# Kernel optimization log

Hardware: AMD Instinct MI355X
Metric: run time of the kernel (lower is better)

The kernel has to match this reference:

```python
import jax, jax.numpy as jnp
import numpy as np

B, CIN, HID, T, W, H, TAU = 8, 16, 64, 4, 32, 32, 5
EPS = 1e-5
DN = ('NCDHW', 'OIDHW', 'NCDHW')


def conv3d(x, w, b):
    # 'same' conv3d, NCDHW layout
    y = jax.lax.conv_general_dilated(x, w, (1, 1, 1), 'SAME', dimension_numbers=DN)
    return y + b[None, :, None, None, None]


def ln3(u):
    # F.layer_norm over the last 3 (spatial) dims, no affine
    mu = jnp.mean(u, axis=(-3, -2, -1), keepdims=True)
    var = jnp.var(u, axis=(-3, -2, -1), keepdims=True)
    return (u - mu) * jax.lax.rsqrt(var + EPS)


def ln4(u, w, b):
    # nn.LayerNorm(memory_shape): over last 4 dims (C,T,W,H), with affine
    mu = jnp.mean(u, axis=(-4, -3, -2, -1), keepdims=True)
    var = jnp.var(u, axis=(-4, -3, -2, -1), keepdims=True)
    return (u - mu) * jax.lax.rsqrt(var + EPS) * w + b


def self_attention(r, c_history):
    scale = 1.0 / np.sqrt(T * W * H)
    scores = jnp.einsum('bctwh,lbctwh->bl', r, c_history) * scale  # [B, TAU]
    # faithful to source: softmax over dim=0 (the batch axis of the [b,l] scores)
    attn = jax.nn.softmax(scores, axis=0)
    return jnp.einsum('bl,lbctwh->bctwh', attn, c_history)


def setup_inputs() -> dict:
    key = jax.random.key(0)
    ks = jax.random.split(key, 8)
    x = jax.random.normal(ks[0], (B, CIN, T, W, H), jnp.float32)
    c_history = jax.random.normal(ks[1], (TAU, B, HID, T, W, H), jnp.float32)
    m = jax.random.normal(ks[2], (B, HID, T, W, H), jnp.float32)
    h = jax.random.normal(ks[3], (B, HID, T, W, H), jnp.float32)
    Wx = jax.random.normal(ks[4], (7, HID, CIN, 3, 3, 3), jnp.float32) * 0.05
    bx = jnp.zeros((7, HID), jnp.float32)
    # 9 state-branch conv kernels: [hr, hi, hg, mi', mg', mf', ho, co, mo]
    Wh = jax.random.normal(ks[5], (9, HID, HID, 3, 3, 3), jnp.float32) * 0.02
    bh = jnp.zeros((9, HID), jnp.float32)
    w111 = jax.random.normal(ks[6], (HID, 2 * HID, 1, 1, 1), jnp.float32) * 0.05
    b111 = jnp.zeros((HID,), jnp.float32)
    ln_w = jnp.ones((HID, T, W, H), jnp.float32)
    ln_b = jnp.zeros((HID, T, W, H), jnp.float32)
    return dict(x=x, c_history=c_history, m=m, h=h, Wx=Wx, bx=bx, Wh=Wh, bh=bh,
                w111=w111, b111=b111, ln_w=ln_w, ln_b=ln_b)


def reference(x, c_history, m, h, Wx, bx, Wh, bh, w111, b111, ln_w, ln_b):
    cx = lambda i: conv3d(x, Wx[i], bx[i])
    cs = lambda u, i: conv3d(u, Wh[i], bh[i])
    r = jax.nn.sigmoid(ln3(cx(0) + cs(h, 0)))
    i = jax.nn.sigmoid(ln3(cx(1) + cs(h, 1)))
    g = jnp.tanh(ln3(cx(2) + cs(h, 2)))
    recall = self_attention(r, c_history)
    c = i * g + ln4(c_history[-1] + recall, ln_w, ln_b)
    i_p = jax.nn.sigmoid(ln3(cx(3) + cs(m, 3)))
    g_p = jnp.tanh(ln3(cx(4) + cs(m, 4)))
    f_p = jax.nn.sigmoid(ln3(cx(5) + cs(m, 5)))
    m_new = i_p * g_p + f_p * m
    o = jax.nn.sigmoid(ln3(cx(6) + cs(h, 6) + cs(c, 7) + cs(m_new, 8)))
    h_new = o * jnp.tanh(conv3d(jnp.concatenate([c, m_new], axis=1), w111, b111))
    c_history_new = jnp.concatenate([c_history[1:], c[None]], axis=0)
    return (c_history_new, m_new, h_new)
```

## Files before the change

kernel.cpp:

```cpp
#include <hip/hip_runtime.h>
#include <hip/hip_bf16.h>
#include <math.h>

#define BATCH 8
#define CIN 16
#define HID 64
#define S2 1024
#define SP 4096
#define CHB 262144
#define TAU 5
#define GATE_SZ 2097152
#define EPS 1e-5f

#define WS_Z_OFF   ((size_t)3 * GATE_SZ)
#define WS_ST_OFF  ((size_t)4 * GATE_SZ)

typedef unsigned short u16;
typedef __attribute__((ext_vector_type(8))) short  short8;
typedef __attribute__((ext_vector_type(8))) u16    ushort8;
typedef __attribute__((ext_vector_type(4))) float  f32x4;

#define N7 (7*27*64*96)
#define NO (27*64*128)
#define N1 (64*128)

__device__ __forceinline__ u16 f2b(float v) {
    __hip_bfloat16 h = __float2bfloat16(v);
    u16 r; __builtin_memcpy(&r, &h, 2); return r;
}

__device__ __forceinline__ float* gate_ptr(float* out, float* ws, int g) {
    return (g < 4) ? (out + (size_t)g * GATE_SZ) : (ws + (size_t)(g - 4) * GATE_SZ);
}

__device__ __forceinline__ float fsig(float v) {
    v = fminf(fmaxf(v, -30.f), 30.f);
    return 1.f / (1.f + __expf(-v));
}
__device__ __forceinline__ float ftanh(float v) {
    v = fminf(fmaxf(v, -15.f), 15.f);
    const float t = __expf(-2.f * v);
    return (1.f - t) / (1.f + t);
}

__global__ __launch_bounds__(256) void pack_w_k(const float* __restrict__ Wx,
                                                const float* __restrict__ Wh,
                                                const float* __restrict__ w111,
                                                u16* __restrict__ A7, u16* __restrict__ Ao,
                                                u16* __restrict__ A111,
                                                float* __restrict__ stats)
{
    if (blockIdx.x == 0 && threadIdx.x < 128) stats[threadIdx.x] = 0.f;
    const int idx = blockIdx.x * 256 + threadIdx.x;
    if (idx < N7) {
        const int k = idx % 96, oc = (idx / 96) % 64, tap = (idx / (96*64)) % 27, g = idx / (96*64*27);
        float v = 0.f;
        if (k < 16)      v = Wx[((size_t)(g*64 + oc)*16 + k)      * 27 + tap];
        else if (k < 80) v = Wh[((size_t)(g*64 + oc)*64 + (k-16)) * 27 + tap];
        A7[idx] = f2b(v);
    } else if (idx < N7 + NO) {
        const int j = idx - N7;
        const int k = j % 128, oc = (j / 128) % 64, tap = j / (128*64);
        float v = (k < 64) ? Wh[((size_t)(7*64 + oc)*64 + k)      * 27 + tap]
                           : Wh[((size_t)(8*64 + oc)*64 + (k-64)) * 27 + tap];
        Ao[j] = f2b(v);
    } else if (idx < N7 + NO + N1) {
        const int j = idx - N7 - NO;
        A111[j] = f2b(w111[j]);
    }
}

__global__ __launch_bounds__(256) void pack_xhm_k(const float* __restrict__ x,
                                                  const float* __restrict__ h,
                                                  const float* __restrict__ m,
                                                  u16* __restrict__ XH, u16* __restrict__ XM)
{
    __shared__ float t[144][65];
    const int bi = blockIdx.x, b = bi >> 6, s0 = (bi & 63) << 6;
    for (int i = threadIdx.x; i < 144*64; i += 256) {
        const int row = i >> 6, sc = i & 63;
        float v;
        if (row < 16)      v = x[((size_t)b*16 + row)      * SP + s0 + sc];
        else if (row < 80) v = h[((size_t)b*64 + (row-16)) * SP + s0 + sc];
        else               v = m[((size_t)b*64 + (row-80)) * SP + s0 + sc];
        t[row][sc] = v;
    }
    __syncthreads();
    for (int j = threadIdx.x; j < 64*96; j += 256) {
        const int s = j / 96, ch = j % 96;
        const size_t o = ((size_t)b*4096 + s0 + s) * 96 + ch;
        XH[o] = f2b(ch < 80 ? t[ch][s] : 0.f);
        XM[o] = f2b(ch < 16 ? t[ch][s] : (ch < 80 ? t[ch + 64][s] : 0.f));
    }
}

__device__ __forceinline__ int swz32(int r, int c) {
    return r * 32 + ((c ^ ((r >> 1) & 3)) << 3);
}

template<int KCH, int TAPS, int NR, int MODE, int MT, int MINW>
__global__ __launch_bounds__(256, MINW) void conv_mfma_k(
    const u16* __restrict__ XA, const u16* __restrict__ XB,
    const u16* __restrict__ Apack,
    const float* __restrict__ bxp, const float* __restrict__ bhp,
    const float* __restrict__ b111,
    float* __restrict__ out, float* __restrict__ ws)
{
    constexpr int YT   = NR + 2;
    constexpr int ROWS = 4 * YT * 34;
    __shared__ __align__(16) u16 xs[ROWS * 32];

    const int bi = blockIdx.x;
    int g = 0, b, y0, ocb = 0, kc_lo = 0, kc_hi = KCH / 32;
    const u16* X; const u16* Ag; float* outp;
    if (MODE == 0) {
        constexpr int YB = 32 / NR;
        ocb = (bi & 1) * 32;
        const int r2 = bi >> 1;
        g  = r2 / (8 * YB);
        b  = (r2 / YB) % 8;
        y0 = (r2 % YB) * NR;
        X  = (g >= 3 && g <= 5) ? XB : XA;
        Ag = Apack + (size_t)g * TAPS * 64 * KCH;
        outp = gate_ptr(out, ws, g) + (size_t)b * CHB;
    } else if (MODE == 1) {
        b = bi >> 5; y0 = bi & 31;
        X = XA; Ag = Apack;
        outp = ws + (size_t)2 * GATE_SZ + (size_t)b * CHB;
    } else {
        b = bi >> 5; y0 = bi & 31;
        X = XA; Ag = Apack;
        outp = ws + (size_t)b * CHB;
    }
    const u16* Xb = X + (size_t)b * 4096 * KCH;

    const int tid  = threadIdx.x;
    const int w    = tid >> 6;
    const int lane = tid & 63;
    const int xn   = lane & 15, quad = lane >> 4;

    f32x4 acc[MT][2 * NR] = {};

    for (int kc = kc_lo; kc < kc_hi; ++kc) {
        if (kc != kc_lo) __syncthreads();
        for (int cix = tid; cix < ROWS * 4; cix += 256) {
            const int r = cix >> 2, sub = cix & 3;
            const int t = r / (YT * 34), rem = r % (YT * 34);
            const int yy = rem / 34, xx = rem % 34;
            const int gy = y0 + yy - 1, gx = xx - 1;
            ushort8 v = {0, 0, 0, 0, 0, 0, 0, 0};
            if ((unsigned)gy < 32u && (unsigned)gx < 32u)
                v = *(const ushort8*)&Xb[(size_t)(t * 1024 + gy * 32 + gx) * KCH + kc * 32 + sub * 8];
            *(ushort8*)&xs[swz32(r, sub)] = v;
        }
        __syncthreads();

        if (TAPS == 27) {
            const int kd_lo = (w == 0) ? 1 : 0;
            const int kd_hi = (w == 3) ? 2 : 3;
            for (int kd = kd_lo; kd < kd_hi; ++kd) {
                const int tin  = w + kd - 1;
                const int rowt = tin * YT * 34;
                #pragma unroll
                for (int jj = 0; jj < 9; ++jj) {
                    const int ky = jj / 3, kx = jj % 3;
                    short8 a[MT], bf[2 * NR];
                    #pragma unroll
                    for (int mt = 0; mt < MT; ++mt)
                        a[mt] = *(const short8*)
                            &Ag[(size_t)((kd * 9 + jj) * 64 + ocb + mt * 16 + xn) * KCH + kc * 32 + quad * 8];
                    #pragma unroll
                    for (int nt = 0; nt < 2 * NR; ++nt) {
                        const int ysub = nt >> 1, xh = nt & 1;
                        const int row = rowt + (ysub + ky) * 34 + xh * 16 + xn + kx;
                        bf[nt] = *(const short8*)&xs[swz32(row, quad)];
                    }
                    #pragma unroll
                    for (int nt = 0; nt < 2 * NR; ++nt)
                        #pragma unroll
                        for (int mt = 0; mt < MT; ++mt)
                            acc[mt][nt] = __builtin_amdgcn_mfma_f32_16x16x32_bf16(a[mt], bf[nt], acc[mt][nt], 0, 0, 0);
                }
            }
        } else {
            short8 a[MT], bf[2 * NR];
            #pragma unroll
            for (int mt = 0; mt < MT; ++mt)
                a[mt] = *(const short8*)&Ag[(size_t)(mt * 16 + xn) * KCH + kc * 32 + quad * 8];
            #pragma unroll
            for (int nt = 0; nt < 2 * NR; ++nt) {
                const int ysub = nt >> 1, xh = nt & 1;
                const int row = (w * YT + ysub + 1) * 34 + xh * 16 + xn + 1;
                bf[nt] = *(const short8*)&xs[swz32(row, quad)];
            }
            #pragma unroll
            for (int nt = 0; nt < 2 * NR; ++nt)
                #pragma unroll
                for (int mt = 0; mt < MT; ++mt)
                    acc[mt][nt] = __builtin_amdgcn_mfma_f32_16x16x32_bf16(a[mt], bf[nt], acc[mt][nt], 0, 0, 0);
        }
    }

    #pragma unroll
    for (int mt = 0; mt < MT; ++mt)
    #pragma unroll
    for (int nt = 0; nt < 2 * NR; ++nt) {
        const int ysub = nt >> 1, xh = nt & 1;
        const int sp = w * 1024 + (y0 + ysub) * 32 + xh * 16 + xn;
        #pragma unroll
        for (int reg = 0; reg < 4; ++reg) {
            const int oc = ocb + mt * 16 + quad * 4 + reg;
            float bias;
            if (MODE == 0)      bias = bxp[g * 64 + oc] + bhp[g * 64 + oc];
            else if (MODE == 1) bias = bhp[7 * 64 + oc] + bhp[8 * 64 + oc];
            else                bias = b111[oc];
            float* p = outp + (size_t)oc * SP + sp;
            float vv = acc[mt][nt][reg] + bias;
            if (MODE == 1) vv += *p;
            *p = vv;
        }
    }
}

__global__ __launch_bounds__(256) void ln3_stats_k(float* __restrict__ out,
                                                   float* __restrict__ ws,
                                                   float* __restrict__ lnstats)
{
    const int blk = blockIdx.x;
    const int g = blk >> 9;
    const float* p = gate_ptr(out, ws, g) + (size_t)(blk & 511) * SP;
    const int tid = threadIdx.x;

    float s = 0.f, s2 = 0.f;
    for (int k = tid; k < SP; k += 256) { float v = p[k]; s += v; s2 += v * v; }
    #pragma unroll
    for (int off = 32; off > 0; off >>= 1) { s += __shfl_down(s, off); s2 += __shfl_down(s2, off); }
    __shared__ float rs[4], rs2[4];
    if ((tid & 63) == 0) { rs[tid >> 6] = s; rs2[tid >> 6] = s2; }
    __syncthreads();
    if (tid == 0) {
        float S  = rs[0] + rs[1] + rs[2] + rs[3];
        float Sq = rs2[0] + rs2[1] + rs2[2] + rs2[3];
        float mu  = S * (1.f / SP);
        float var = Sq * (1.f / SP) - mu * mu;
        lnstats[2 * blk]     = mu;
        lnstats[2 * blk + 1] = rsqrtf(var + EPS);
    }
}

__global__ __launch_bounds__(256) void ln3_act_k(float* __restrict__ out,
                                                 float* __restrict__ ws, int gate0)
{
    const int blk = blockIdx.x;
    const int g = gate0 + (blk >> 9);
    float* p = gate_ptr(out, ws, g) + (size_t)(blk & 511) * SP;
    const int tid = threadIdx.x;

    float s = 0.f, s2 = 0.f;
    for (int k = tid; k < SP; k += 256) { float v = p[k]; s += v; s2 += v * v; }
    #pragma unroll
    for (int off = 32; off > 0; off >>= 1) { s += __shfl_down(s, off); s2 += __shfl_down(s2, off); }
    __shared__ float rs[4], rs2[4], stat[2];
    if ((tid & 63) == 0) { rs[tid >> 6] = s; rs2[tid >> 6] = s2; }
    __syncthreads();
    if (tid == 0) {
        float S  = rs[0] + rs[1] + rs[2] + rs[3];
        float Sq = rs2[0] + rs2[1] + rs2[2] + rs2[3];
        float mu  = S * (1.f / SP);
        float var = Sq * (1.f / SP) - mu * mu;
        stat[0] = mu; stat[1] = rsqrtf(var + EPS);
    }
    __syncthreads();
    const float mu = stat[0], r = stat[1];
    for (int k = tid; k < SP; k += 256)
        p[k] = fsig((p[k] - mu) * r);
}

__global__ __launch_bounds__(256) void scores_k(const float* __restrict__ u0,
                                                const float* __restrict__ chist,
                                                const float* __restrict__ lnstats,
                                                float* __restrict__ stats)
{
    const int blk = blockIdx.x;
    const int b = blk >> 6, chn = blk & 63;
    const float mu = lnstats[2 * (b * 64 + chn)];
    const float rr = lnstats[2 * (b * 64 + chn) + 1];
    const float* rp = u0 + (size_t)b * CHB;
    const int lo = chn * SP;
    float s[TAU] = {};
    for (int k = lo + threadIdx.x; k < lo + SP; k += 256) {
        const float rv = fsig((rp[k] - mu) * rr);
        #pragma unroll
        for (int l = 0; l < TAU; ++l) s[l] += rv * chist[(size_t)(l * BATCH + b) * CHB + k];
    }
    __shared__ float rsh[TAU][4];
    #pragma unroll
    for (int l = 0; l < TAU; ++l) {
        float v = s[l];
        #pragma unroll
        for (int off = 32; off > 0; off >>= 1) v += __shfl_down(v, off);
        if ((threadIdx.x & 63) == 0) rsh[l][threadIdx.x >> 6] = v;
    }
    __syncthreads();
    if (threadIdx.x < TAU) {
        const int l = threadIdx.x;
        atomicAdd(&stats[l * 8 + b],
                  (rsh[l][0] + rsh[l][1] + rsh[l][2] + rsh[l][3]) * (1.f / 64.f));
    }
}

__global__ __launch_bounds__(256) void recall_k(const float* __restrict__ chist,
                                                float* __restrict__ ws,
                                                float* __restrict__ part)
{
    const float* stats = ws + WS_ST_OFF;
    const int blk = blockIdx.x;
    const int b = blk >> 10;
    const int idx = (blk & 1023) * 256 + threadIdx.x;

    __shared__ float attn[TAU];
    if (threadIdx.x < TAU) {
        const int l = threadIdx.x;
        float mx = -1e30f;
        for (int bb = 0; bb < BATCH; ++bb) mx = fmaxf(mx, stats[l * 8 + bb]);
        float sum = 0.f, e = 0.f;
        for (int bb = 0; bb < BATCH; ++bb) {
            float t = __expf(stats[l * 8 + bb] - mx);
            sum += t;
            if (bb == b) e = t;
        }
        attn[l] = e / sum;
    }
    __syncthreads();
    const float a0 = attn[0], a1 = attn[1], a2 = attn[2], a3 = attn[3], a4 = attn[4];

    const size_t e = (size_t)b * CHB + idx;
    const size_t LB = (size_t)BATCH * CHB;
    float z = chist[4 * LB + e] * (1.f + a4)
            + a0 * chist[0 * LB + e] + a1 * chist[1 * LB + e]
            + a2 * chist[2 * LB + e] + a3 * chist[3 * LB + e];
    ws[WS_Z_OFF + e] = z;

    float s = z, s2 = z * z;
    #pragma unroll
    for (int off = 32; off > 0; off >>= 1) { s += __shfl_down(s, off); s2 += __shfl_down(s2, off); }
    __shared__ float rs[4], rs2[4];
    if ((threadIdx.x & 63) == 0) { rs[threadIdx.x >> 6] = s; rs2[threadIdx.x >> 6] = s2; }
    __syncthreads();
    if (threadIdx.x == 0) {
        part[blk]        = rs[0] + rs[1] + rs[2] + rs[3];
        part[8192 + blk] = rs2[0] + rs2[1] + rs2[2] + rs2[3];
    }
}

__global__ __launch_bounds__(256) void cm_pcm_k(float* __restrict__ out, float* __restrict__ ws,
                                                const float* __restrict__ m,
                                                const float* __restrict__ lnw,
                                                const float* __restrict__ lnb,
                                                const float* __restrict__ part,
                                                const float* __restrict__ lnstats,
                                                u16* __restrict__ PCM)
{
    __shared__ __align__(16) u16 tl[64][136];
    __shared__ float lst[5][64][2];
    const int bi = blockIdx.x;
    const int b = bi >> 6;
    const int s0 = (bi & 63) << 6;

    for (int j = threadIdx.x; j < 5 * 64; j += 256) {
        const int gg = j >> 6, chn = j & 63;
        lst[gg][chn][0] = lnstats[2 * ((gg + 1) * 512 + b * 64 + chn)];
        lst[gg][chn][1] = lnstats[2 * ((gg + 1) * 512 + b * 64 + chn) + 1];
    }
    float s = 0.f, s2 = 0.f;
    for (int j = threadIdx.x; j < 1024; j += 256) {
        s  += part[b * 1024 + j];
        s2 += part[8192 + b * 1024 + j];
    }
    #pragma unroll
    for (int off = 32; off > 0; off >>= 1) { s += __shfl_down(s, off); s2 += __shfl_down(s2, off); }
    __shared__ float rs[4], rs2[4], st[2];
    if ((threadIdx.x & 63) == 0) { rs[threadIdx.x >> 6] = s; rs2[threadIdx.x >> 6] = s2; }
    __syncthreads();
    if (threadIdx.x == 0) {
        float S  = rs[0] + rs[1] + rs[2] + rs[3];
        float Sq = rs2[0] + rs2[1] + rs2[2] + rs2[3];
        float mu  = S * (1.f / CHB);
        float var = Sq * (1.f / CHB) - mu * mu;
        st[0] = mu; st[1] = rsqrtf(var + EPS);
    }
    __syncthreads();
    const float mu = st[0], rstd = st[1];

    for (int i = threadIdx.x; i < 1024; i += 256) {
        const int chn = i >> 4;
        const int sp4 = (i & 15) << 2;
        const size_t e = (size_t)b * CHB + (size_t)chn * SP + s0 + sp4;
        const size_t le = (size_t)chn * SP + s0 + sp4;
        float4 z  = *(const float4*)&ws[WS_Z_OFF + e];
        float4 u1 = *(const float4*)&gate_ptr(out, ws, 1)[e];
        float4 u2 = *(const float4*)&gate_ptr(out, ws, 2)[e];
        float4 u3 = *(const float4*)&gate_ptr(out, ws, 3)[e];
        float4 u4 = *(const float4*)&gate_ptr(out, ws, 4)[e];
        float4 u5 = *(const float4*)&gate_ptr(out, ws, 5)[e];
        float4 mm = *(const float4*)&m[e];
        float4 lw = *(const float4*)&lnw[le];
        float4 lb = *(const float4*)&lnb[le];
        const float m1 = lst[0][chn][0], r1 = lst[0][chn][1];
        const float m2 = lst[1][chn][0], r2 = lst[1][chn][1];
        const float m3 = lst[2][chn][0], r3 = lst[2][chn][1];
        const float m4 = lst[3][chn][0], r4 = lst[3][chn][1];
        const float m5 = lst[4][chn][0], r5 = lst[4][chn][1];
        float4 c, mn;
        {
            const float uu1[4] = {u1.x, u1.y, u1.z, u1.w};
            const float uu2[4] = {u2.x, u2.y, u2.z, u2.w};
            const float uu3[4] = {u3.x, u3.y, u3.z, u3.w};
            const float uu4[4] = {u4.x, u4.y, u4.z, u4.w};
            const float uu5[4] = {u5.x, u5.y, u5.z, u5.w};
            const float zz[4]  = {z.x, z.y, z.z, z.w};
            const float mmv[4] = {mm.x, mm.y, mm.z, mm.w};
            const float lwv[4] = {lw.x, lw.y, lw.z, lw.w};
            const float lbv[4] = {lb.x, lb.y, lb.z, lb.w};
            float cv[4], mv[4];
            #pragma unroll
            for (int k = 0; k < 4; ++k) {
                const float gi = fsig ((uu1[k] - m1) * r1);
                const float gg = ftanh((uu2[k] - m2) * r2);
                const float ip = fsig ((uu3[k] - m3) * r3);
                const float gp = ftanh((uu4[k] - m4) * r4);
                const float fp = fsig ((uu5[k] - m5) * r5);
                cv[k] = gi * gg + (zz[k] - mu) * rstd * lwv[k] + lbv[k];
                mv[k] = ip * gp + fp * mmv[k];
                tl[sp4 + k][chn]      = f2b(cv[k]);
                tl[sp4 + k][64 + chn] = f2b(mv[k]);
            }
            c.x = cv[0]; c.y = cv[1]; c.z = cv[2]; c.w = cv[3];
            mn.x = mv[0]; mn.y = mv[1]; mn.z = mv[2]; mn.w = mv[3];
        }
        *(float4*)&out[(size_t)4 * GATE_SZ + e] = c;
        *(float4*)&out[(size_t)5 * GATE_SZ + e] = mn;
    }
    __syncthreads();
    for (int j = threadIdx.x; j < 1024; j += 256) {
        const int sidx = j >> 4, c8 = (j & 15) << 3;
        ushort8 v = *(const ushort8*)&tl[sidx][c8];
        *(ushort8*)&PCM[((size_t)b * 4096 + s0 + sidx) * 128 + c8] = v;
    }
}

__global__ __launch_bounds__(256) void tail_k(const float* __restrict__ chist,
                                              const float* __restrict__ o,
                                              const float* __restrict__ v,
                                              float* __restrict__ out)
{
    const int bi = blockIdx.x;
    if (bi < 8192) {
        const size_t i = (size_t)bi * 256 + threadIdx.x;
        ((float4*)out)[i] = ((const float4*)(chist + GATE_SZ))[i];
    } else {
        const size_t i = (size_t)(bi - 8192) * 256 + threadIdx.x;
        float4 ov = ((const float4*)o)[i], vv = ((const float4*)v)[i];
        float4 r;
        r.x = ov.x * ftanh(vv.x); r.y = ov.y * ftanh(vv.y);
        r.z = ov.z * ftanh(vv.z); r.w = ov.w * ftanh(vv.w);
        ((float4*)(out + (size_t)6 * GATE_SZ))[i] = r;
    }
}

extern "C" void kernel_launch(void* const* d_in, const int* in_sizes, int n_in,
                              void* d_out, int out_size, void* d_ws, size_t ws_size,
                              hipStream_t stream)
{
    const float* x    = (const float*)d_in[0];
    const float* ch   = (const float*)d_in[1];
    const float* m    = (const float*)d_in[2];
    const float* h    = (const float*)d_in[3];
    const float* Wx   = (const float*)d_in[4];
    const float* bx   = (const float*)d_in[5];
    const float* Wh   = (const float*)d_in[6];
    const float* bh   = (const float*)d_in[7];
    const float* w111 = (const float*)d_in[8];
    const float* b111 = (const float*)d_in[9];
    const float* lnw  = (const float*)d_in[10];
    const float* lnb  = (const float*)d_in[11];
    float* out = (float*)d_out;
    float* ws  = (float*)d_ws;

    u16* XH   = (u16*)(out + (size_t)4 * GATE_SZ);
    u16* A7   = (u16*)(out + (size_t)5 * GATE_SZ);
    u16* XM   = (u16*)(out + (size_t)6 * GATE_SZ);
    u16* Ao   = XM + (size_t)BATCH * 4096 * 96;
    u16* A111 = Ao + (size_t)NO;
    u16* PCM  = (u16*)out;
    float* part    = (float*)(A111 + N1);
    float* lnstats = part + 16384;
    float* stats   = ws + WS_ST_OFF;

    pack_w_k<<<(N7 + NO + N1 + 255) / 256, 256, 0, stream>>>(Wx, Wh, w111, A7, Ao, A111, stats);
    pack_xhm_k<<<512, 256, 0, stream>>>(x, h, m, XH, XM);

    conv_mfma_k<96, 27, 2, 0, 2, 4><<<1792, 256, 0, stream>>>(XH, XM, A7, bx, bh, nullptr, out, ws);
    ln3_stats_k<<<3072, 256, 0, stream>>>(out, ws, lnstats);

    scores_k<<<512, 256, 0, stream>>>(out, ch, lnstats, stats);
    recall_k<<<8192, 256, 0, stream>>>(ch, ws, part);
    cm_pcm_k<<<512, 256, 0, stream>>>(out, ws, m, lnw, lnb, part, lnstats, PCM);

    conv_mfma_k<128, 27, 1, 1, 4, 3><<<256, 256, 0, stream>>>(PCM, nullptr, Ao, nullptr, bh, nullptr, out, ws);
    ln3_act_k<<<512, 256, 0, stream>>>(out, ws, 6);
    conv_mfma_k<128, 1, 1, 2, 4, 3><<<256, 256, 0, stream>>>(PCM, nullptr, A111, nullptr, nullptr, b111, out, ws);

    tail_k<<<10240, 256, 0, stream>>>(ch, ws + (size_t)2 * GATE_SZ, ws, out);
}
```

Before: 392.1 us.

## Fuse LN3 stats into conv epilogue via atomics and double-buffer tap loads

```diff
diff --git a/kernel.cpp b/kernel.cpp
--- a/kernel.cpp
+++ b/kernel.cpp
@@ -48,10 +48,12 @@
                                                 const float* __restrict__ w111,
                                                 u16* __restrict__ A7, u16* __restrict__ Ao,
                                                 u16* __restrict__ A111,
-                                                float* __restrict__ stats)
-{
-    if (blockIdx.x == 0 && threadIdx.x < 128) stats[threadIdx.x] = 0.f;
+                                                float* __restrict__ stats,
+                                                float* __restrict__ sums)
+{
     const int idx = blockIdx.x * 256 + threadIdx.x;
+    if (idx < 128)  stats[idx] = 0.f;
+    if (idx < 6144) sums[idx] = 0.f;
     if (idx < N7) {
         const int k = idx % 96, oc = (idx / 96) % 64, tap = (idx / (96*64)) % 27, g = idx / (96*64*27);
         float v = 0.f;
@@ -104,7 +106,8 @@
     const u16* __restrict__ Apack,
     const float* __restrict__ bxp, const float* __restrict__ bhp,
     const float* __restrict__ b111,
-    float* __restrict__ out, float* __restrict__ ws)
+    float* __restrict__ out, float* __restrict__ ws,
+    float* __restrict__ sums)
 {
     constexpr int YT   = NR + 2;
     constexpr int ROWS = 4 * YT * 34;
@@ -155,49 +158,48 @@
         }
         __syncthreads();
 
-        if (TAPS == 27) {
-            const int kd_lo = (w == 0) ? 1 : 0;
-            const int kd_hi = (w == 3) ? 2 : 3;
-            for (int kd = kd_lo; kd < kd_hi; ++kd) {
-                const int tin  = w + kd - 1;
-                const int rowt = tin * YT * 34;
-                #pragma unroll
-                for (int jj = 0; jj < 9; ++jj) {
-                    const int ky = jj / 3, kx = jj % 3;
-                    short8 a[MT], bf[2 * NR];
-                    #pragma unroll
-                    for (int mt = 0; mt < MT; ++mt)
-                        a[mt] = *(const short8*)
-                            &Ag[(size_t)((kd * 9 + jj) * 64 + ocb + mt * 16 + xn) * KCH + kc * 32 + quad * 8];
-                    #pragma unroll
-                    for (int nt = 0; nt < 2 * NR; ++nt) {
-                        const int ysub = nt >> 1, xh = nt & 1;
-                        const int row = rowt + (ysub + ky) * 34 + xh * 16 + xn + kx;
-                        bf[nt] = *(const short8*)&xs[swz32(row, quad)];
-                    }
-                    #pragma unroll
-                    for (int nt = 0; nt < 2 * NR; ++nt)
-                        #pragma unroll
-                        for (int mt = 0; mt < MT; ++mt)
-                            acc[mt][nt] = __builtin_amdgcn_mfma_f32_16x16x32_bf16(a[mt], bf[nt], acc[mt][nt], 0, 0, 0);
-                }
-            }
-        } else {
-            short8 a[MT], bf[2 * NR];
+        auto load_ab = [&](short8* a, short8* bf, int kd_, int ky_, int kx_) {
+            const int tap = (TAPS == 27) ? (kd_ * 9 + ky_ * 3 + kx_) : 0;
             #pragma unroll
             for (int mt = 0; mt < MT; ++mt)
-                a[mt] = *(const short8*)&Ag[(size_t)(mt * 16 + xn) * KCH + kc * 32 + quad * 8];
+                a[mt] = *(const short8*)
+                    &Ag[(size_t)(tap * 64 + ocb + mt * 16 + xn) * KCH + kc * 32 + quad * 8];
+            const int rowt = (w + kd_ - 1) * YT * 34;
             #pragma unroll
             for (int nt = 0; nt < 2 * NR; ++nt) {
                 const int ysub = nt >> 1, xh = nt & 1;
-                const int row = (w * YT + ysub + 1) * 34 + xh * 16 + xn + 1;
+                const int row = rowt + (ysub + ky_) * 34 + xh * 16 + xn + kx_;
                 bf[nt] = *(const short8*)&xs[swz32(row, quad)];
             }
+        };
+        auto do_mfma = [&](short8* a, short8* bf) {
             #pragma unroll
             for (int nt = 0; nt < 2 * NR; ++nt)
                 #pragma unroll
                 for (int mt = 0; mt < MT; ++mt)
                     acc[mt][nt] = __builtin_amdgcn_mfma_f32_16x16x32_bf16(a[mt], bf[nt], acc[mt][nt], 0, 0, 0);
+        };
+
+        if (TAPS == 27) {
+            int kd = (w == 0) ? 1 : 0;
+            const int kd_hi = (w == 3) ? 2 : 3;
+            const int ntap = (kd_hi - kd) * 9;
+            int ky = 0, kx = 0;
+            auto adv = [&]() { if (++kx == 3) { kx = 0; if (++ky == 3) { ky = 0; ++kd; } } };
+
+            short8 a0[MT], b0[2 * NR], a1[MT], b1[2 * NR];
+            load_ab(a0, b0, kd, ky, kx);
+            for (int t = 0; t + 2 <= ntap; t += 2) {
+                adv(); load_ab(a1, b1, kd, ky, kx);
+                do_mfma(a0, b0);
+                if (t + 3 <= ntap) { adv(); load_ab(a0, b0, kd, ky, kx); }
+                do_mfma(a1, b1);
+            }
+            if (ntap & 1) do_mfma(a0, b0);
+        } else {
+            short8 a0[MT], b0[2 * NR];
+            load_ab(a0, b0, 1, 1, 1);
+            do_mfma(a0, b0);
         }
     }
 
@@ -220,31 +222,31 @@
             *p = vv;
         }
     }
-}
-
-__global__ __launch_bounds__(256) void ln3_stats_k(float* __restrict__ out,
-                                                   float* __restrict__ ws,
-                                                   float* __restrict__ lnstats)
-{
-    const int blk = blockIdx.x;
-    const int g = blk >> 9;
-    const float* p = gate_ptr(out, ws, g) + (size_t)(blk & 511) * SP;
-    const int tid = threadIdx.x;
-
-    float s = 0.f, s2 = 0.f;
-    for (int k = tid; k < SP; k += 256) { float v = p[k]; s += v; s2 += v * v; }
-    #pragma unroll
-    for (int off = 32; off > 0; off >>= 1) { s += __shfl_down(s, off); s2 += __shfl_down(s2, off); }
-    __shared__ float rs[4], rs2[4];
-    if ((tid & 63) == 0) { rs[tid >> 6] = s; rs2[tid >> 6] = s2; }
-    __syncthreads();
-    if (tid == 0) {
-        float S  = rs[0] + rs[1] + rs[2] + rs[3];
-        float Sq = rs2[0] + rs2[1] + rs2[2] + rs2[3];
-        float mu  = S * (1.f / SP);
-        float var = Sq * (1.f / SP) - mu * mu;
-        lnstats[2 * blk]     = mu;
-        lnstats[2 * blk + 1] = rsqrtf(var + EPS);
+
+    if (MODE == 0 && g < 6) {
+        #pragma unroll
+        for (int mt = 0; mt < MT; ++mt)
+        #pragma unroll
+        for (int reg = 0; reg < 4; ++reg) {
+            const int oc = ocb + mt * 16 + quad * 4 + reg;
+            const float bias = bxp[g * 64 + oc] + bhp[g * 64 + oc];
+            float s = 0.f, s2 = 0.f;
+            #pragma unroll
+            for (int nt = 0; nt < 2 * NR; ++nt) {
+                const float vv = acc[mt][nt][reg] + bias;
+                s += vv; s2 += vv * vv;
+            }
+            #pragma unroll
+            for (int off = 8; off > 0; off >>= 1) {
+                s  += __shfl_xor(s, off);
+                s2 += __shfl_xor(s2, off);
+            }
+            if (xn == 0) {
+                float* dst = &sums[(size_t)((g * 8 + b) * 64 + oc) * 2];
+                atomicAdd(dst, s);
+                atomicAdd(dst + 1, s2);
+            }
+        }
     }
 }
 
@@ -278,13 +280,15 @@
 
 __global__ __launch_bounds__(256) void scores_k(const float* __restrict__ u0,
                                                 const float* __restrict__ chist,
-                                                const float* __restrict__ lnstats,
+                                                const float* __restrict__ sums,
                                                 float* __restrict__ stats)
 {
     const int blk = blockIdx.x;
     const int b = blk >> 6, chn = blk & 63;
-    const float mu = lnstats[2 * (b * 64 + chn)];
-    const float rr = lnstats[2 * (b * 64 + chn) + 1];
+    const float* sp2 = &sums[(size_t)(b * 64 + chn) * 2];
+    const float mu = sp2[0] * (1.f / SP);
+    const float var = sp2[1] * (1.f / SP) - mu * mu;
+    const float rr = rsqrtf(var + EPS);
     const float* rp = u0 + (size_t)b * CHB;
     const int lo = chn * SP;
     float s[TAU] = {};
@@ -358,7 +362,7 @@
                                                 const float* __restrict__ lnw,
                                                 const float* __restrict__ lnb,
                                                 const float* __restrict__ part,
-                                                const float* __restrict__ lnstats,
+                                                const float* __restrict__ sums,
                                                 u16* __restrict__ PCM)
 {
     __shared__ __align__(16) u16 tl[64][136];
@@ -369,8 +373,11 @@
 
     for (int j = threadIdx.x; j < 5 * 64; j += 256) {
         const int gg = j >> 6, chn = j & 63;
-        lst[gg][chn][0] = lnstats[2 * ((gg + 1) * 512 + b * 64 + chn)];
-        lst[gg][chn][1] = lnstats[2 * ((gg + 1) * 512 + b * 64 + chn) + 1];
+        const float* sp2 = &sums[(size_t)(((gg + 1) * 8 + b) * 64 + chn) * 2];
+        const float mu_ = sp2[0] * (1.f / SP);
+        const float var_ = sp2[1] * (1.f / SP) - mu_ * mu_;
+        lst[gg][chn][0] = mu_;
+        lst[gg][chn][1] = rsqrtf(var_ + EPS);
     }
     float s = 0.f, s2 = 0.f;
     for (int j = threadIdx.x; j < 1024; j += 256) {
@@ -493,23 +500,22 @@
     u16* Ao   = XM + (size_t)BATCH * 4096 * 96;
     u16* A111 = Ao + (size_t)NO;
     u16* PCM  = (u16*)out;
-    float* part    = (float*)(A111 + N1);
-    float* lnstats = part + 16384;
-    float* stats   = ws + WS_ST_OFF;
-
-    pack_w_k<<<(N7 + NO + N1 + 255) / 256, 256, 0, stream>>>(Wx, Wh, w111, A7, Ao, A111, stats);
+    float* part = (float*)(A111 + N1);
+    float* sums = part + 16384;
+    float* stats = ws + WS_ST_OFF;
+
+    pack_w_k<<<(N7 + NO + N1 + 255) / 256, 256, 0, stream>>>(Wx, Wh, w111, A7, Ao, A111, stats, sums);
     pack_xhm_k<<<512, 256, 0, stream>>>(x, h, m, XH, XM);
 
-    conv_mfma_k<96, 27, 2, 0, 2, 4><<<1792, 256, 0, stream>>>(XH, XM, A7, bx, bh, nullptr, out, ws);
-    ln3_stats_k<<<3072, 256, 0, stream>>>(out, ws, lnstats);
-
-    scores_k<<<512, 256, 0, stream>>>(out, ch, lnstats, stats);
+    conv_mfma_k<96, 27, 2, 0, 2, 4><<<1792, 256, 0, stream>>>(XH, XM, A7, bx, bh, nullptr, out, ws, sums);
+
+    scores_k<<<512, 256, 0, stream>>>(out, ch, sums, stats);
     recall_k<<<8192, 256, 0, stream>>>(ch, ws, part);
-    cm_pcm_k<<<512, 256, 0, stream>>>(out, ws, m, lnw, lnb, part, lnstats, PCM);
-
-    conv_mfma_k<128, 27, 1, 1, 4, 3><<<256, 256, 0, stream>>>(PCM, nullptr, Ao, nullptr, bh, nullptr, out, ws);
+    cm_pcm_k<<<512, 256, 0, stream>>>(out, ws, m, lnw, lnb, part, sums, PCM);
+
+    conv_mfma_k<128, 27, 1, 1, 4, 3><<<256, 256, 0, stream>>>(PCM, nullptr, Ao, nullptr, bh, nullptr, out, ws, nullptr);
     ln3_act_k<<<512, 256, 0, stream>>>(out, ws, 6);
-    conv_mfma_k<128, 1, 1, 2, 4, 3><<<256, 256, 0, stream>>>(PCM, nullptr, A111, nullptr, nullptr, b111, out, ws);
+    conv_mfma_k<128, 1, 1, 2, 4, 3><<<256, 256, 0, stream>>>(PCM, nullptr, A111, nullptr, nullptr, b111, out, ws, nullptr);
 
     tail_k<<<10240, 256, 0, stream>>>(ch, ws + (size_t)2 * GATE_SZ, ws, out);
 }
```

Measured after the change: 402.7 us. 1.03x slower.

## Rebalance conv output-channel split, pad LDS rows, software-pipeline tap loads

Applied to the files above, without the earlier changes.

```diff
diff --git a/kernel.cpp b/kernel.cpp
--- a/kernel.cpp
+++ b/kernel.cpp
@@ -50,8 +50,8 @@
                                                 u16* __restrict__ A111,
                                                 float* __restrict__ stats)
 {
-    if (blockIdx.x == 0 && threadIdx.x < 128) stats[threadIdx.x] = 0.f;
     const int idx = blockIdx.x * 256 + threadIdx.x;
+    if (idx < 128) stats[idx] = 0.f;
     if (idx < N7) {
         const int k = idx % 96, oc = (idx / 96) % 64, tap = (idx / (96*64)) % 27, g = idx / (96*64*27);
         float v = 0.f;
@@ -94,10 +94,6 @@
     }
 }
 
-__device__ __forceinline__ int swz32(int r, int c) {
-    return r * 32 + ((c ^ ((r >> 1) & 3)) << 3);
-}
-
 template<int KCH, int TAPS, int NR, int MODE, int MT, int MINW>
 __global__ __launch_bounds__(256, MINW) void conv_mfma_k(
     const u16* __restrict__ XA, const u16* __restrict__ XB,
@@ -108,23 +104,24 @@
 {
     constexpr int YT   = NR + 2;
     constexpr int ROWS = 4 * YT * 34;
-    __shared__ __align__(16) u16 xs[ROWS * 32];
+    constexpr int PADK = 40;
+    __shared__ __align__(16) u16 xs[ROWS * PADK];
 
     const int bi = blockIdx.x;
-    int g = 0, b, y0, ocb = 0, kc_lo = 0, kc_hi = KCH / 32;
+    int g = 0, b, y0, ocb = 0;
     const u16* X; const u16* Ag; float* outp;
     if (MODE == 0) {
         constexpr int YB = 32 / NR;
-        ocb = (bi & 1) * 32;
-        const int r2 = bi >> 1;
-        g  = r2 / (8 * YB);
-        b  = (r2 / YB) % 8;
-        y0 = (r2 % YB) * NR;
+        g  = bi / (8 * YB);
+        b  = (bi / YB) % 8;
+        y0 = (bi % YB) * NR;
         X  = (g >= 3 && g <= 5) ? XB : XA;
         Ag = Apack + (size_t)g * TAPS * 64 * KCH;
         outp = gate_ptr(out, ws, g) + (size_t)b * CHB;
     } else if (MODE == 1) {
-        b = bi >> 5; y0 = bi & 31;
+        ocb = (bi & 1) * 32;
+        b  = bi >> 6;
+        y0 = (bi >> 1) & 31;
         X = XA; Ag = Apack;
         outp = ws + (size_t)2 * GATE_SZ + (size_t)b * CHB;
     } else {
@@ -141,8 +138,8 @@
 
     f32x4 acc[MT][2 * NR] = {};
 
-    for (int kc = kc_lo; kc < kc_hi; ++kc) {
-        if (kc != kc_lo) __syncthreads();
+    for (int kc = 0; kc < KCH / 32; ++kc) {
+        if (kc != 0) __syncthreads();
         for (int cix = tid; cix < ROWS * 4; cix += 256) {
             const int r = cix >> 2, sub = cix & 3;
             const int t = r / (YT * 34), rem = r % (YT * 34);
@@ -151,53 +148,53 @@
             ushort8 v = {0, 0, 0, 0, 0, 0, 0, 0};
             if ((unsigned)gy < 32u && (unsigned)gx < 32u)
                 v = *(const ushort8*)&Xb[(size_t)(t * 1024 + gy * 32 + gx) * KCH + kc * 32 + sub * 8];
-            *(ushort8*)&xs[swz32(r, sub)] = v;
+            *(ushort8*)&xs[r * PADK + sub * 8] = v;
         }
         __syncthreads();
 
-        if (TAPS == 27) {
-            const int kd_lo = (w == 0) ? 1 : 0;
-            const int kd_hi = (w == 3) ? 2 : 3;
-            for (int kd = kd_lo; kd < kd_hi; ++kd) {
-                const int tin  = w + kd - 1;
-                const int rowt = tin * YT * 34;
-                #pragma unroll
-                for (int jj = 0; jj < 9; ++jj) {
-                    const int ky = jj / 3, kx = jj % 3;
-                    short8 a[MT], bf[2 * NR];
-                    #pragma unroll
-                    for (int mt = 0; mt < MT; ++mt)
-                        a[mt] = *(const short8*)
-                            &Ag[(size_t)((kd * 9 + jj) * 64 + ocb + mt * 16 + xn) * KCH + kc * 32 + quad * 8];
-                    #pragma unroll
-                    for (int nt = 0; nt < 2 * NR; ++nt) {
-                        const int ysub = nt >> 1, xh = nt & 1;
-                        const int row = rowt + (ysub + ky) * 34 + xh * 16 + xn + kx;
-                        bf[nt] = *(const short8*)&xs[swz32(row, quad)];
-                    }
-                    #pragma unroll
-                    for (int nt = 0; nt < 2 * NR; ++nt)
-                        #pragma unroll
-                        for (int mt = 0; mt < MT; ++mt)
-                            acc[mt][nt] = __builtin_amdgcn_mfma_f32_16x16x32_bf16(a[mt], bf[nt], acc[mt][nt], 0, 0, 0);
-                }
-            }
-        } else {
-            short8 a[MT], bf[2 * NR];
+        auto load_a = [&](short8* a, int tap) {
             #pragma unroll
             for (int mt = 0; mt < MT; ++mt)
-                a[mt] = *(const short8*)&Ag[(size_t)(mt * 16 + xn) * KCH + kc * 32 + quad * 8];
+                a[mt] = *(const short8*)
+                    &Ag[(size_t)(tap * 64 + ocb + mt * 16 + xn) * KCH + kc * 32 + quad * 8];
+        };
+        auto load_b = [&](short8* bf, int tap) {
+            int kd, ky, kx;
+            if (TAPS == 27) { kd = tap / 9; ky = (tap / 3) % 3; kx = tap % 3; }
+            else            { kd = 1; ky = 1; kx = 1; }
+            const int tin = w + kd - 1;
             #pragma unroll
             for (int nt = 0; nt < 2 * NR; ++nt) {
                 const int ysub = nt >> 1, xh = nt & 1;
-                const int row = (w * YT + ysub + 1) * 34 + xh * 16 + xn + 1;
-                bf[nt] = *(const short8*)&xs[swz32(row, quad)];
+                bf[nt] = *(const short8*)
+                    &xs[((tin * YT + ysub + ky) * 34 + xh * 16 + xn + kx) * PADK + quad * 8];
             }
+        };
+        auto do_mfma = [&](short8* a, short8* bf) {
             #pragma unroll
             for (int nt = 0; nt < 2 * NR; ++nt)
                 #pragma unroll
                 for (int mt = 0; mt < MT; ++mt)
                     acc[mt][nt] = __builtin_amdgcn_mfma_f32_16x16x32_bf16(a[mt], bf[nt], acc[mt][nt], 0, 0, 0);
+        };
+
+        if (TAPS == 27) {
+            const int tap_lo = (w == 0) ? 9 : 0;
+            const int tap_hi = (w == 3) ? 18 : 27;
+            short8 a0[MT], b0[2 * NR], a1[MT], b1[2 * NR];
+            load_a(a0, tap_lo); load_b(b0, tap_lo);
+            int tap = tap_lo;
+            for (; tap + 2 <= tap_hi; tap += 2) {
+                load_a(a1, tap + 1); load_b(b1, tap + 1);
+                do_mfma(a0, b0);
+                if (tap + 2 < tap_hi) { load_a(a0, tap + 2); load_b(b0, tap + 2); }
+                do_mfma(a1, b1);
+            }
+            if (tap < tap_hi) do_mfma(a0, b0);
+        } else {
+            short8 a0[MT], b0[2 * NR];
+            load_a(a0, 0); load_b(b0, 0);
+            do_mfma(a0, b0);
         }
     }
 
@@ -500,14 +497,14 @@
     pack_w_k<<<(N7 + NO + N1 + 255) / 256, 256, 0, stream>>>(Wx, Wh, w111, A7, Ao, A111, stats);
     pack_xhm_k<<<512, 256, 0, stream>>>(x, h, m, XH, XM);
 
-    conv_mfma_k<96, 27, 2, 0, 2, 4><<<1792, 256, 0, stream>>>(XH, XM, A7, bx, bh, nullptr, out, ws);
+    conv_mfma_k<96, 27, 2, 0, 4, 3><<<896, 256, 0, stream>>>(XH, XM, A7, bx, bh, nullptr, out, ws);
     ln3_stats_k<<<3072, 256, 0, stream>>>(out, ws, lnstats);
 
     scores_k<<<512, 256, 0, stream>>>(out, ch, lnstats, stats);
     recall_k<<<8192, 256, 0, stream>>>(ch, ws, part);
     cm_pcm_k<<<512, 256, 0, stream>>>(out, ws, m, lnw, lnb, part, lnstats, PCM);
 
-    conv_mfma_k<128, 27, 1, 1, 4, 3><<<256, 256, 0, stream>>>(PCM, nullptr, Ao, nullptr, bh, nullptr, out, ws);
+    conv_mfma_k<128, 27, 1, 1, 2, 4><<<512, 256, 0, stream>>>(PCM, nullptr, Ao, nullptr, bh, nullptr, out, ws);
     ln3_act_k<<<512, 256, 0, stream>>>(out, ws, 6);
     conv_mfma_k<128, 1, 1, 2, 4, 3><<<256, 256, 0, stream>>>(PCM, nullptr, A111, nullptr, nullptr, b111, out, ws);
 
```

New measurement: 386.7 us. About the same (-1.4%).
